# Kernel tuning notes

Measured on AMD Instinct MI355X. Metric: run time of the kernel, lower is better.

## Reference

```python
import jax, jax.numpy as jnp
import numpy as np

OFFSET = (0, 0)
STRIDE = (2, 2)

B, C, H, W = 2, 256, 384, 384
N_ACTIVE = 16384
GRID = 192  # strided index grid: OFFSET + (GRID-1)*STRIDE < H


def setup_inputs() -> dict:
    key = jax.random.key(0)
    k1, k2, k3 = jax.random.split(key, 3)
    x = jax.random.normal(k1, (B, C, N_ACTIVE), dtype=jnp.float32)
    original_output = jax.random.normal(k2, (B, C, H, W), dtype=jnp.float32)
    active_indices = jax.random.randint(k3, (N_ACTIVE, 2), 0, GRID, dtype=jnp.int32)
    return {"x": x, "original_output": original_output, "active_indices": active_indices}


def reference(x, original_output, active_indices):
    # Scatter-write active values into the dense output at strided/offset coords.
    # write location for active index k: (OFFSET[0] + iy*STRIDE[0], OFFSET[1] + ix*STRIDE[1])
    h = OFFSET[0] + active_indices[:, 0] * STRIDE[0]  # [N]
    w = OFFSET[1] + active_indices[:, 1] * STRIDE[1]  # [N]
    # advanced indexing on the two spatial dims -> [B, C, N] slots, overwritten by x
    out = original_output.at[:, :, h, w].set(x)
    return out
```

## Files before the change

kernel.cpp:

```cpp
#include <hip/hip_runtime.h>

#define BB      2
#define CC      256
#define HH      384
#define WW      384
#define N_ACT   16384
#define GRID_N  192
#define PLANE_F4 ((HH * WW) / 4)
#define ROW_F4   (WW / 4)

__global__ void init_winner_kernel(int* __restrict__ winner) {
    int i = blockIdx.x * blockDim.x + threadIdx.x;
    if (i < GRID_N * GRID_N) winner[i] = -1;
}

__global__ void winner_scatter_kernel(const int* __restrict__ idx,
                                      int* __restrict__ winner) {
    int k = blockIdx.x * blockDim.x + threadIdx.x;
    if (k < N_ACT) {
        int iy = idx[2 * k];
        int ix = idx[2 * k + 1];
        atomicMax(&winner[iy * GRID_N + ix], k);
    }
}

__global__ void scatter_main_kernel(const float4* __restrict__ orig,
                                    const float* __restrict__ x,
                                    const int* __restrict__ winner,
                                    float4* __restrict__ out) {
    int bc  = blockIdx.y;
    int rem = blockIdx.x * blockDim.x + threadIdx.x;
    long long base = (long long)bc * PLANE_F4 + rem;

    float4 v = orig[base];

    int y  = rem / ROW_F4;
    int x4 = rem - y * ROW_F4;

    if ((y & 1) == 0) {
        int gy = y >> 1;
        int gx = x4 << 1;
        const int* wrow = winner + gy * GRID_N;
        int w0 = wrow[gx];
        int w1 = wrow[gx + 1];
        const float* xp = x + (long long)bc * N_ACT;
        if (w0 >= 0) v.x = xp[w0];
        if (w1 >= 0) v.z = xp[w1];
    }

    out[base] = v;
}

extern "C" void kernel_launch(void* const* d_in, const int* in_sizes, int n_in,
                              void* d_out, int out_size, void* d_ws, size_t ws_size,
                              hipStream_t stream) {
    const float* x    = (const float*)d_in[0];
    const float* orig = (const float*)d_in[1];
    const int*   idx  = (const int*)d_in[2];
    float*       out  = (float*)d_out;
    int*         winner = (int*)d_ws;

    init_winner_kernel<<<dim3((GRID_N * GRID_N + 255) / 256), dim3(256), 0, stream>>>(winner);
    winner_scatter_kernel<<<dim3((N_ACT + 255) / 256), dim3(256), 0, stream>>>(idx, winner);
    scatter_main_kernel<<<dim3(PLANE_F4 / 256, BB * CC), dim3(256), 0, stream>>>(
        (const float4*)orig, x, winner, (float4*)out);
}
```

Measured before the change: 143.9 us.

## Process row pairs per thread with nontemporal loads/stores and memset init

Each thread now handles one even row float4 and the odd row float4 below it, so every thread does the winner lookup and the half of threads that did no scatter work are gone. The copy uses nontemporal loads and stores to stream the large plane data past the caches. The init kernel is replaced by hipMemsetAsync to 0xFF, and the winner row is read as a single int2. The risk is that a memset may cost about as much as a tiny kernel, and nontemporal hints can change bandwidth either way.

```diff
diff --git a/kernel.cpp b/kernel.cpp
--- a/kernel.cpp
+++ b/kernel.cpp
@@ -8,11 +8,9 @@
 #define GRID_N  192
 #define PLANE_F4 ((HH * WW) / 4)
 #define ROW_F4   (WW / 4)
+#define PAIRS_PER_PLANE (PLANE_F4 / 2)
 
-__global__ void init_winner_kernel(int* __restrict__ winner) {
-    int i = blockIdx.x * blockDim.x + threadIdx.x;
-    if (i < GRID_N * GRID_N) winner[i] = -1;
-}
+typedef float  fx4 __attribute__((ext_vector_type(4)));
 
 __global__ void winner_scatter_kernel(const int* __restrict__ idx,
                                       int* __restrict__ winner) {
@@ -24,31 +22,30 @@
     }
 }
 
-__global__ void scatter_main_kernel(const float4* __restrict__ orig,
+__global__ void scatter_main_kernel(const fx4* __restrict__ orig,
                                     const float* __restrict__ x,
                                     const int* __restrict__ winner,
-                                    float4* __restrict__ out) {
-    int bc  = blockIdx.y;
-    int rem = blockIdx.x * blockDim.x + threadIdx.x;
-    long long base = (long long)bc * PLANE_F4 + rem;
+                                    fx4* __restrict__ out) {
+    int bc = blockIdx.y;
+    int q  = blockIdx.x * blockDim.x + threadIdx.x;
+    int gy  = q / ROW_F4;
+    int col = q - gy * ROW_F4;
 
-    float4 v = orig[base];
+    int base = bc * PLANE_F4 + (gy * 2) * ROW_F4 + col;
 
-    int y  = rem / ROW_F4;
-    int x4 = rem - y * ROW_F4;
+    fx4 ve = __builtin_nontemporal_load(&orig[base]);
+    fx4 vo = __builtin_nontemporal_load(&orig[base + ROW_F4]);
+    const int2* wrow2 = reinterpret_cast<const int2*>(winner + gy * GRID_N);
+    int2 w = wrow2[col];
 
-    if ((y & 1) == 0) {
-        int gy = y >> 1;
-        int gx = x4 << 1;
-        const int* wrow = winner + gy * GRID_N;
-        int w0 = wrow[gx];
-        int w1 = wrow[gx + 1];
-        const float* xp = x + (long long)bc * N_ACT;
-        if (w0 >= 0) v.x = xp[w0];
-        if (w1 >= 0) v.z = xp[w1];
+    if (w.x >= 0 || w.y >= 0) {
+        const float* xp = x + bc * N_ACT;
+        if (w.x >= 0) ve[0] = xp[w.x];
+        if (w.y >= 0) ve[2] = xp[w.y];
     }
 
-    out[base] = v;
+    __builtin_nontemporal_store(ve, &out[base]);
+    __builtin_nontemporal_store(vo, &out[base + ROW_F4]);
 }
 
 extern "C" void kernel_launch(void* const* d_in, const int* in_sizes, int n_in,
@@ -60,8 +57,8 @@
     float*       out  = (float*)d_out;
     int*         winner = (int*)d_ws;
 
-    init_winner_kernel<<<dim3((GRID_N * GRID_N + 255) / 256), dim3(256), 0, stream>>>(winner);
+    (void)hipMemsetAsync(winner, 0xFF, GRID_N * GRID_N * sizeof(int), stream);
     winner_scatter_kernel<<<dim3((N_ACT + 255) / 256), dim3(256), 0, stream>>>(idx, winner);
-    scatter_main_kernel<<<dim3(PLANE_F4 / 256, BB * CC), dim3(256), 0, stream>>>(
-        (const float4*)orig, x, winner, (float4*)out);
+    scatter_main_kernel<<<dim3(PAIRS_PER_PLANE / 256, BB * CC), dim3(256), 0, stream>>>(
+        (const fx4*)orig, x, winner, (fx4*)out);
 }
```

New measurement: 135.7 us. -5.7%, faster.
